# Kernel optimization log

Measured on AMD Instinct MI355X. Metric: run time of the kernel, lower is better.

Reference implementation:

```python
import jax, jax.numpy as jnp
import numpy as np

IN_C, HID, L, NN, BS, OUT = 32, 128, 4, 64, 512, 3
N = NN * BS  # total graph vertices
EPS_LN = 1e-5
EPS_SM = 1e-16  # PyG softmax eps


def setup_inputs() -> dict:
    key = jax.random.key(0)
    ks = jax.random.split(key, 16)
    E = 524288
    x = jax.random.normal(ks[0], (N, IN_C), dtype=jnp.float32)
    edge_index = jax.random.randint(ks[1], (2, E), 0, N, dtype=jnp.int64)
    s = 0.1
    # first GAT layer (in -> hidden)
    W0 = jax.random.normal(ks[2], (IN_C, HID), dtype=jnp.float32) * s
    att_src0 = jax.random.normal(ks[3], (HID,), dtype=jnp.float32) * s
    att_dst0 = jax.random.normal(ks[4], (HID,), dtype=jnp.float32) * s
    bias0 = jnp.zeros((HID,), dtype=jnp.float32)
    # residual GAT layers (hidden -> hidden), stacked over L
    W_res = jax.random.normal(ks[5], (L, HID, HID), dtype=jnp.float32) * s
    att_src_res = jax.random.normal(ks[6], (L, HID), dtype=jnp.float32) * s
    att_dst_res = jax.random.normal(ks[7], (L, HID), dtype=jnp.float32) * s
    bias_res = jnp.zeros((L, HID), dtype=jnp.float32)
    gamma = jnp.ones((L, HID), dtype=jnp.float32)
    beta = jnp.zeros((L, HID), dtype=jnp.float32)
    # per-node predictor heads
    W1p = jax.random.normal(ks[8], (NN, HID, HID // 2), dtype=jnp.float32) * s
    W2p = jax.random.normal(ks[9], (NN, HID // 2, OUT), dtype=jnp.float32) * s
    return {"x": x, "edge_index": edge_index, "W0": W0, "att_src0": att_src0,
            "att_dst0": att_dst0, "bias0": bias0, "W_res": W_res,
            "att_src_res": att_src_res, "att_dst_res": att_dst_res,
            "bias_res": bias_res, "gamma": gamma, "beta": beta,
            "W1p": W1p, "W2p": W2p}


def _gat(x, src, dst, W, a_src, a_dst, b):
    # PyG GATConv, heads=1, negative_slope=0.2, self-loops already appended
    h = x @ W                                   # [N, H]
    a_s = (h * a_src).sum(-1)                   # [N]
    a_d = (h * a_dst).sum(-1)                   # [N]
    e = jax.nn.leaky_relu(a_s[src] + a_d[dst], 0.2)   # [E]
    m = jax.ops.segment_max(e, dst, num_segments=N)
    e = jnp.exp(e - m[dst])
    z = jax.ops.segment_sum(e, dst, num_segments=N)
    alpha = e / (z[dst] + EPS_SM)               # [E]
    out = jax.ops.segment_sum(h[src] * alpha[:, None], dst, num_segments=N)
    return out + b


def _layernorm(x, g, b):
    mu = x.mean(-1, keepdims=True)
    var = ((x - mu) ** 2).mean(-1, keepdims=True)
    return (x - mu) * jax.lax.rsqrt(var + EPS_LN) * g + b


def reference(x, edge_index, W0, att_src0, att_dst0, bias0, W_res,
              att_src_res, att_dst_res, bias_res, gamma, beta, W1p, W2p):
    loops = jnp.arange(N, dtype=edge_index.dtype)
    src = jnp.concatenate([edge_index[0], loops])
    dst = jnp.concatenate([edge_index[1], loops])
    # first GAT + relu
    h = jax.nn.relu(_gat(x, src, dst, W0, att_src0, att_dst0, bias0))
    # res+ blocks: h = h + conv(dropout(act(norm(h))))  (dropout=identity, eval)
    for i in range(L):
        t = jax.nn.relu(_layernorm(h, gamma[i], beta[i]))
        t = _gat(t, src, dst, W_res[i], att_src_res[i], att_dst_res[i], bias_res[i])
        h = h + t
    h = jax.nn.relu(_layernorm(h, gamma[0], beta[0]))
    # per-node predictor heads
    h = h.reshape(NN, BS, HID)
    t = jax.nn.relu(jnp.einsum('nbh,nhk->nbk', h, W1p))
    logits = jnp.einsum('nbk,nko->nbo', t, W2p)
    return jax.nn.softmax(logits, axis=-1)   # softmax over class dim (dim=1 per node slice)
```

## Files before the change

### kernel.cpp

```cpp
#include <hip/hip_runtime.h>
#include <math.h>

#define NND   32768
#define HIDD  128
#define NHEAD 64
#define BSS   512
#define OUTC  3

typedef _Float16 half_t;
typedef __attribute__((ext_vector_type(8))) _Float16 half8;
typedef __attribute__((ext_vector_type(4))) float f32x4;

__global__ __launch_bounds__(256) void prep_kernel(const float* __restrict__ W0,
        const float* __restrict__ W_res, const float* __restrict__ W1p,
        const float* __restrict__ as0, const float* __restrict__ ad0,
        const float* __restrict__ as_res, const float* __restrict__ ad_res,
        const float* __restrict__ x,
        half_t* __restrict__ Wh, half_t* __restrict__ W1h, half_t* __restrict__ W0t,
        float* __restrict__ wvec, half_t* __restrict__ xh, int* __restrict__ counts) {
    int b = blockIdx.x, tid = threadIdx.x;
    if (b < 64) {
        __shared__ float tile[32][33];
        int l = b >> 4, t = b & 15;
        int k0 = (t >> 2) * 32, n0 = (t & 3) * 32;
        const float* src = W_res + (size_t)l * 128 * 128;
        half_t* dst = Wh + (size_t)l * 128 * 128;
        int c = tid & 31, r0 = tid >> 5;
#pragma unroll
        for (int i = 0; i < 4; ++i) tile[r0 + i * 8][c] = src[(size_t)(k0 + r0 + i * 8) * 128 + n0 + c];
        __syncthreads();
#pragma unroll
        for (int i = 0; i < 4; ++i) dst[(size_t)(n0 + r0 + i * 8) * 128 + k0 + c] = (half_t)tile[c][r0 + i * 8];
    } else if (b < 576) {
        __shared__ float tile[32][33];
        int bb = b - 64, head = bb >> 3, t = bb & 7;
        int k0 = (t >> 1) * 32, n0 = (t & 1) * 32;
        const float* src = W1p + (size_t)head * 128 * 64;
        half_t* dst = W1h + (size_t)head * 64 * 128;
        int c = tid & 31, r0 = tid >> 5;
#pragma unroll
        for (int i = 0; i < 4; ++i) tile[r0 + i * 8][c] = src[(size_t)(k0 + r0 + i * 8) * 64 + n0 + c];
        __syncthreads();
#pragma unroll
        for (int i = 0; i < 4; ++i) dst[(size_t)(n0 + r0 + i * 8) * 128 + k0 + c] = (half_t)tile[c][r0 + i * 8];
    } else if (b == 576) {
        __shared__ float t0[32][129];
        for (int i = tid; i < 4096; i += 256) t0[i >> 7][i & 127] = W0[i];
        __syncthreads();
        for (int i = tid; i < 4096; i += 256) { int n = i >> 5, k = i & 31; W0t[n * 32 + k] = (half_t)t0[k][n]; }
    } else if (b == 577) {
        for (int task = tid; task < 1088; task += 256) {
            const float* row; const float* att; int slot, sd;
            if (task < 64) {
                int k = task >> 1; sd = task & 1;
                row = W0 + k * 128; att = sd ? ad0 : as0; slot = k;
            } else {
                int tt = task - 64; int l = 1 + tt / 256; int r = tt % 256;
                int k = r >> 1; sd = r & 1;
                row = W_res + (size_t)(l - 1) * 16384 + k * 128;
                att = (sd ? ad_res : as_res) + (l - 1) * 128;
                slot = l * 128 + k;
            }
            float s = 0.f;
            for (int n = 0; n < 128; ++n) s += row[n] * att[n];
            (sd ? wvec + 640 : wvec)[slot] = s;
        }
    } else if (b < 1090) {
        int b2 = b - 578;
        const float* xs = x + (size_t)b2 * 64 * 32;
        half_t* xd = xh + (size_t)b2 * 64 * 32;
        for (int i = tid; i < 1024; i += 256) {
            float2 v = ((const float2*)xs)[i];
            union { unsigned u; half_t h[2]; } cv;
            cv.h[0] = (half_t)v.x; cv.h[1] = (half_t)v.y;
            ((unsigned*)xd)[i] = cv.u;
        }
    } else {
        int b3 = b - 1090;
        ((int4*)counts)[b3 * 256 + tid] = make_int4(0, 0, 0, 0);
    }
}

__global__ __launch_bounds__(256) void a0_kernel(const half_t* __restrict__ xh,
                                                 const float* __restrict__ wvec,
                                                 float* __restrict__ a_s, float* __restrict__ a_d) {
    __shared__ float ws0[32], wd0[32];
    int tid = threadIdx.x;
    if (tid < 32) { ws0[tid] = wvec[tid]; wd0[tid] = wvec[640 + tid]; }
    __syncthreads();
    int g = blockIdx.x * 256 + tid;
    int node = g >> 2, part = g & 3;
    half8 xv = *(const half8*)&xh[(size_t)node * 32 + part * 8];
    float s = 0.f, d2 = 0.f;
#pragma unroll
    for (int j = 0; j < 8; ++j) { float f = (float)xv[j]; s += f * ws0[part * 8 + j]; d2 += f * wd0[part * 8 + j]; }
    s += __shfl_xor(s, 1); s += __shfl_xor(s, 2);
    d2 += __shfl_xor(d2, 1); d2 += __shfl_xor(d2, 2);
    if (part == 0) { a_s[node] = s; a_d[node] = d2; }
}

__global__ void count_kernel(const int* __restrict__ ei, int E,
                             int* __restrict__ counts, int* __restrict__ rank) {
    int j = blockIdx.x * 256 + threadIdx.x;
    int Etot = E + NND;
    if (j >= Etot) return;
    int dst = (j < E) ? ei[E + j] : (j - E);
    rank[j] = atomicAdd(&counts[dst], 1);
}

__global__ __launch_bounds__(1024) void scan_kernel(const int* __restrict__ counts,
                                                    int* __restrict__ off) {
    __shared__ int sums[1024];
    int tid = threadIdx.x;
    int base = tid * 32;
    int tmp[32];
    int run = 0;
#pragma unroll
    for (int i = 0; i < 8; ++i) {
        int4 c4 = *(const int4*)&counts[base + i * 4];
        tmp[i*4+0] = run; run += c4.x;
        tmp[i*4+1] = run; run += c4.y;
        tmp[i*4+2] = run; run += c4.z;
        tmp[i*4+3] = run; run += c4.w;
    }
    sums[tid] = run;
    __syncthreads();
    for (int d = 1; d < 1024; d <<= 1) {
        int v = (tid >= d) ? sums[tid - d] : 0;
        __syncthreads();
        sums[tid] += v;
        __syncthreads();
    }
    int ebase = (tid == 0) ? 0 : sums[tid - 1];
#pragma unroll
    for (int i = 0; i < 32; ++i) off[base + i] = ebase + tmp[i];
    if (tid == 1023) off[NND] = sums[1023];
}

__global__ void fill_kernel(const int* __restrict__ ei, int E,
                            const int* __restrict__ off, const int* __restrict__ rank,
                            int* __restrict__ csr_src) {
    int j = blockIdx.x * 256 + threadIdx.x;
    int Etot = E + NND;
    if (j >= Etot) return;
    int src, dst;
    if (j < E) { src = ei[j]; dst = ei[E + j]; }
    else       { src = j - E; dst = j - E; }
    csr_src[off[dst] + rank[j]] = src;
}

__global__ __launch_bounds__(256) void agg0_kernel(const half_t* __restrict__ xh,
        const float* __restrict__ a_s, const float* __restrict__ a_dv,
        const int* __restrict__ csr_src, const int* __restrict__ off,
        half_t* __restrict__ P) {
    int d = (blockIdx.x * 256 + threadIdx.x) >> 6;
    int lane = threadIdx.x & 63;
    int q = lane >> 4, r15 = lane & 15;
    int beg = off[d], end = off[d + 1];
    float adv = a_dv[d];
    float pz = 0.f, a0 = 0.f, a1 = 0.f;
    for (int base = beg; base < end; base += 64) {
        int j = base + lane;
        int s = 0; float p = 0.f;
        if (j < end) {
            s = csr_src[j];
            float t = a_s[s] + adv;
            t = (t > 0.f) ? t : 0.2f * t;
            p = __expf(t);
        }
        pz += p;
        int cnt = end - base; if (cnt > 64) cnt = 64;
        int full = cnt & ~15;
        int k4 = 0;
        for (; k4 < full; k4 += 16) {
            int s0 = __shfl(s, k4 + q);      float p0 = __shfl(p, k4 + q);
            int s1 = __shfl(s, k4 + 4 + q);  float p1 = __shfl(p, k4 + 4 + q);
            int s2 = __shfl(s, k4 + 8 + q);  float p2 = __shfl(p, k4 + 8 + q);
            int s3 = __shfl(s, k4 + 12 + q); float p3 = __shfl(p, k4 + 12 + q);
            union { unsigned u; half_t h[2]; } u0, u1, u2, u3;
            u0.u = *(const unsigned*)&xh[(size_t)s0 * 32 + r15 * 2];
            u1.u = *(const unsigned*)&xh[(size_t)s1 * 32 + r15 * 2];
            u2.u = *(const unsigned*)&xh[(size_t)s2 * 32 + r15 * 2];
            u3.u = *(const unsigned*)&xh[(size_t)s3 * 32 + r15 * 2];
            a0 += p0 * (float)u0.h[0] + p1 * (float)u1.h[0] + p2 * (float)u2.h[0] + p3 * (float)u3.h[0];
            a1 += p0 * (float)u0.h[1] + p1 * (float)u1.h[1] + p2 * (float)u2.h[1] + p3 * (float)u3.h[1];
        }
        for (; k4 < cnt; k4 += 4) {
            int s0 = __shfl(s, k4 + q); float p0 = __shfl(p, k4 + q);
            union { unsigned u; half_t h[2]; } u0;
            u0.u = *(const unsigned*)&xh[(size_t)s0 * 32 + r15 * 2];
            a0 += p0 * (float)u0.h[0]; a1 += p0 * (float)u0.h[1];
        }
    }
#pragma unroll
    for (int o = 32; o; o >>= 1) pz += __shfl_xor(pz, o);
    a0 += __shfl_xor(a0, 16); a0 += __shfl_xor(a0, 32);
    a1 += __shfl_xor(a1, 16); a1 += __shfl_xor(a1, 32);
    if (q == 0) {
        float inv = 1.f / (pz + 1e-16f);
        union { unsigned u; half_t h[2]; } w;
        w.h[0] = (half_t)(a0 * inv); w.h[1] = (half_t)(a1 * inv);
        *(unsigned*)&P[(size_t)d * 32 + r15 * 2] = w.u;
    }
}

__global__ __launch_bounds__(256) void agg_kernel(const half_t* __restrict__ F,
        const float* __restrict__ a_s, const float* __restrict__ a_dv,
        const int* __restrict__ csr_src, const int* __restrict__ off,
        half_t* __restrict__ P) {
    int d = (blockIdx.x * 256 + threadIdx.x) >> 6;
    int lane = threadIdx.x & 63;
    int q = lane >> 4, r15 = lane & 15;
    int beg = off[d], end = off[d + 1];
    float adv = a_dv[d];
    float pz = 0.f;
    float acc[8] = {0.f,0.f,0.f,0.f,0.f,0.f,0.f,0.f};
    for (int base = beg; base < end; base += 64) {
        int j = base + lane;
        int s = 0; float p = 0.f;
        if (j < end) {
            s = csr_src[j];
            float t = a_s[s] + adv;
            t = (t > 0.f) ? t : 0.2f * t;
            p = __expf(t);
        }
        pz += p;
        int cnt = end - base; if (cnt > 64) cnt = 64;
        int full = cnt & ~15;
        int k4 = 0;
        for (; k4 < full; k4 += 16) {
            int s0 = __shfl(s, k4 + q);      float p0 = __shfl(p, k4 + q);
            int s1 = __shfl(s, k4 + 4 + q);  float p1 = __shfl(p, k4 + 4 + q);
            int s2 = __shfl(s, k4 + 8 + q);  float p2 = __shfl(p, k4 + 8 + q);
            int s3 = __shfl(s, k4 + 12 + q); float p3 = __shfl(p, k4 + 12 + q);
            half8 h0 = *(const half8*)&F[(size_t)s0 * HIDD + r15 * 8];
            half8 h1 = *(const half8*)&F[(size_t)s1 * HIDD + r15 * 8];
            half8 h2 = *(const half8*)&F[(size_t)s2 * HIDD + r15 * 8];
            half8 h3 = *(const half8*)&F[(size_t)s3 * HIDD + r15 * 8];
#pragma unroll
            for (int i = 0; i < 8; ++i) acc[i] += p0 * (float)h0[i];
#pragma unroll
            for (int i = 0; i < 8; ++i) acc[i] += p1 * (float)h1[i];
#pragma unroll
            for (int i = 0; i < 8; ++i) acc[i] += p2 * (float)h2[i];
#pragma unroll
            for (int i = 0; i < 8; ++i) acc[i] += p3 * (float)h3[i];
        }
        for (; k4 < cnt; k4 += 4) {
            int s0 = __shfl(s, k4 + q); float p0 = __shfl(p, k4 + q);
            half8 h0 = *(const half8*)&F[(size_t)s0 * HIDD + r15 * 8];
#pragma unroll
            for (int i = 0; i < 8; ++i) acc[i] += p0 * (float)h0[i];
        }
    }
#pragma unroll
    for (int o = 32; o; o >>= 1) pz += __shfl_xor(pz, o);
#pragma unroll
    for (int i = 0; i < 8; ++i) {
        acc[i] += __shfl_xor(acc[i], 16);
        acc[i] += __shfl_xor(acc[i], 32);
    }
    if (q == 0) {
        float inv = 1.f / (pz + 1e-16f);
        union { int4 v; half_t hh[8]; } u;
#pragma unroll
        for (int i = 0; i < 8; ++i) u.hh[i] = (half_t)(acc[i] * inv);
        *(int4*)&P[(size_t)d * HIDD + r15 * 8] = u.v;
    }
}

template <int K, bool RES>
__global__ __launch_bounds__(256) void gemm_kernel(const half_t* __restrict__ P,
        const half_t* __restrict__ Whl, const float* __restrict__ bias,
        float* __restrict__ Hbuf, half_t* __restrict__ Th,
        const float* __restrict__ gamma, const float* __restrict__ beta,
        const float* __restrict__ wsn, const float* __restrict__ wdn,
        float* __restrict__ a_s, float* __restrict__ a_d) {
    constexpr int KP = K + 8;
    __shared__ half_t Wt[128 * KP];
    __shared__ half_t OutT[64 * HIDD];
    int tid = threadIdx.x;
    int n0 = blockIdx.x * 64;
    for (int i = tid; i < 128 * (K / 8); i += 256) {
        int n = i / (K / 8), c = i % (K / 8);
        *(int4*)&Wt[n * KP + c * 8] = *(const int4*)&Whl[(size_t)n * K + c * 8];
    }
    int wv = tid >> 6, lane = tid & 63;
    int q = lane >> 4, r15 = lane & 15;
    half8 afrag[K / 32];
    int nodeA = n0 + wv * 16 + r15;
#pragma unroll
    for (int s = 0; s < K / 32; ++s)
        afrag[s] = *(const half8*)&P[(size_t)nodeA * K + s * 32 + q * 8];
    __syncthreads();
    f32x4 acc[8];
#pragma unroll
    for (int ct = 0; ct < 8; ++ct) {
        f32x4 c = {0.f, 0.f, 0.f, 0.f};
#pragma unroll
        for (int s = 0; s < K / 32; ++s) {
            half8 bfrag = *(const half8*)&Wt[(ct * 16 + r15) * KP + s * 32 + q * 8];
            c = __builtin_amdgcn_mfma_f32_16x16x32_f16(afrag[s], bfrag, c, 0, 0, 0);
        }
        acc[ct] = c;
    }
    int nodeD = n0 + wv * 16 + q * 4;
    float v[8][4];
#pragma unroll
    for (int ct = 0; ct < 8; ++ct) {
        int ch = ct * 16 + r15;
        float bv = bias[ch];
#pragma unroll
        for (int r = 0; r < 4; ++r) {
            float x2 = acc[ct][r] + bv;
            if (RES) x2 += Hbuf[(size_t)(nodeD + r) * HIDD + ch];
            else     x2 = fmaxf(x2, 0.f);
            v[ct][r] = x2;
            Hbuf[(size_t)(nodeD + r) * HIDD + ch] = x2;
        }
    }
    float sum[4] = {0.f,0.f,0.f,0.f};
#pragma unroll
    for (int ct = 0; ct < 8; ++ct)
#pragma unroll
        for (int r = 0; r < 4; ++r) sum[r] += v[ct][r];
#pragma unroll
    for (int o = 8; o; o >>= 1)
#pragma unroll
        for (int r = 0; r < 4; ++r) sum[r] += __shfl_xor(sum[r], o);
    float mu[4], var[4] = {0.f,0.f,0.f,0.f};
#pragma unroll
    for (int r = 0; r < 4; ++r) mu[r] = sum[r] * (1.f / HIDD);
#pragma unroll
    for (int ct = 0; ct < 8; ++ct)
#pragma unroll
        for (int r = 0; r < 4; ++r) { float dx = v[ct][r] - mu[r]; var[r] += dx * dx; }
#pragma unroll
    for (int o = 8; o; o >>= 1)
#pragma unroll
        for (int r = 0; r < 4; ++r) var[r] += __shfl_xor(var[r], o);
    float rs[4];
#pragma unroll
    for (int r = 0; r < 4; ++r) rs[r] = rsqrtf(var[r] * (1.f / HIDD) + 1e-5f);
    float asn[4] = {0.f,0.f,0.f,0.f}, adn[4] = {0.f,0.f,0.f,0.f};
#pragma unroll
    for (int ct = 0; ct < 8; ++ct) {
        int ch = ct * 16 + r15;
        float g = gamma[ch], be = beta[ch], wsv = wsn[ch], wdv = wdn[ch];
#pragma unroll
        for (int r = 0; r < 4; ++r) {
            float t = fmaxf((v[ct][r] - mu[r]) * rs[r] * g + be, 0.f);
            OutT[(wv * 16 + q * 4 + r) * HIDD + ch] = (half_t)t;
            asn[r] += t * wsv;
            adn[r] += t * wdv;
        }
    }
#pragma unroll
    for (int o = 8; o; o >>= 1)
#pragma unroll
        for (int r = 0; r < 4; ++r) { asn[r] += __shfl_xor(asn[r], o); adn[r] += __shfl_xor(adn[r], o); }
    if (r15 == 0) {
#pragma unroll
        for (int r = 0; r < 4; ++r) { a_s[nodeD + r] = asn[r]; a_d[nodeD + r] = adn[r]; }
    }
    __syncthreads();
    const int4* srcp = (const int4*)OutT;
    int4* dstp = (int4*)&Th[(size_t)n0 * HIDD];
    for (int i = tid; i < 64 * HIDD * 2 / 16; i += 256)
        dstp[i] = srcp[i];
}

__global__ __launch_bounds__(256) void gemm_last_kernel(const half_t* __restrict__ P,
        const half_t* __restrict__ Whl, const float* __restrict__ bias,
        const float* __restrict__ Hbuf,
        const float* __restrict__ gamma, const float* __restrict__ beta,
        const half_t* __restrict__ W1h, const float* __restrict__ W2p,
        float* __restrict__ out) {
    __shared__ half_t Wt[128 * 136];
    __shared__ half_t OutT[64 * HIDD];
    int tid = threadIdx.x;
    int n0 = blockIdx.x * 64;
    for (int i = tid; i < 128 * 16; i += 256) {
        int n = i >> 4, c = i & 15;
        *(int4*)&Wt[n * 136 + c * 8] = *(const int4*)&Whl[(size_t)n * 128 + c * 8];
    }
    int wv = tid >> 6, lane = tid & 63;
    int q = lane >> 4, r15 = lane & 15;
    half8 afrag[4];
    int nodeA = n0 + wv * 16 + r15;
#pragma unroll
    for (int s = 0; s < 4; ++s)
        afrag[s] = *(const half8*)&P[(size_t)nodeA * HIDD + s * 32 + q * 8];
    __syncthreads();
    f32x4 acc[8];
#pragma unroll
    for (int ct = 0; ct < 8; ++ct) {
        f32x4 c = {0.f, 0.f, 0.f, 0.f};
#pragma unroll
        for (int s = 0; s < 4; ++s) {
            half8 bfrag = *(const half8*)&Wt[(ct * 16 + r15) * 136 + s * 32 + q * 8];
            c = __builtin_amdgcn_mfma_f32_16x16x32_f16(afrag[s], bfrag, c, 0, 0, 0);
        }
        acc[ct] = c;
    }
    int nodeD = n0 + wv * 16 + q * 4;
    float v[8][4];
#pragma unroll
    for (int ct = 0; ct < 8; ++ct) {
        int ch = ct * 16 + r15;
        float bv = bias[ch];
#pragma unroll
        for (int r = 0; r < 4; ++r)
            v[ct][r] = acc[ct][r] + bv + Hbuf[(size_t)(nodeD + r) * HIDD + ch];
    }
    float sum[4] = {0.f,0.f,0.f,0.f};
#pragma unroll
    for (int ct = 0; ct < 8; ++ct)
#pragma unroll
        for (int r = 0; r < 4; ++r) sum[r] += v[ct][r];
#pragma unroll
    for (int o = 8; o; o >>= 1)
#pragma unroll
        for (int r = 0; r < 4; ++r) sum[r] += __shfl_xor(sum[r], o);
    float mu[4], var[4] = {0.f,0.f,0.f,0.f};
#pragma unroll
    for (int r = 0; r < 4; ++r) mu[r] = sum[r] * (1.f / HIDD);
#pragma unroll
    for (int ct = 0; ct < 8; ++ct)
#pragma unroll
        for (int r = 0; r < 4; ++r) { float dx = v[ct][r] - mu[r]; var[r] += dx * dx; }
#pragma unroll
    for (int o = 8; o; o >>= 1)
#pragma unroll
        for (int r = 0; r < 4; ++r) var[r] += __shfl_xor(var[r], o);
    float rs[4];
#pragma unroll
    for (int r = 0; r < 4; ++r) rs[r] = rsqrtf(var[r] * (1.f / HIDD) + 1e-5f);
#pragma unroll
    for (int ct = 0; ct < 8; ++ct) {
        int ch = ct * 16 + r15;
        float g = gamma[ch], be = beta[ch];
#pragma unroll
        for (int r = 0; r < 4; ++r) {
            float t = fmaxf((v[ct][r] - mu[r]) * rs[r] * g + be, 0.f);
            OutT[(wv * 16 + q * 4 + r) * HIDD + ch] = (half_t)t;
        }
    }
    __syncthreads();
    int head = n0 >> 9;
    const half_t* W1g = W1h + (size_t)head * 64 * 128;
    half8 pa[4];
#pragma unroll
    for (int s = 0; s < 4; ++s)
        pa[s] = *(const half8*)&OutT[(wv * 16 + r15) * HIDD + s * 32 + q * 8];
    float lg[3][4];
#pragma unroll
    for (int o = 0; o < 3; ++o)
#pragma unroll
        for (int r = 0; r < 4; ++r) lg[o][r] = 0.f;
#pragma unroll
    for (int ct2 = 0; ct2 < 4; ++ct2) {
        int n2 = ct2 * 16 + r15;
        f32x4 c = {0.f, 0.f, 0.f, 0.f};
#pragma unroll
        for (int s = 0; s < 4; ++s) {
            half8 bfrag = *(const half8*)&W1g[(size_t)n2 * 128 + s * 32 + q * 8];
            c = __builtin_amdgcn_mfma_f32_16x16x32_f16(pa[s], bfrag, c, 0, 0, 0);
        }
        float w2a = W2p[(size_t)head * 192 + n2 * 3 + 0];
        float w2b = W2p[(size_t)head * 192 + n2 * 3 + 1];
        float w2c = W2p[(size_t)head * 192 + n2 * 3 + 2];
#pragma unroll
        for (int r = 0; r < 4; ++r) {
            float t = fmaxf(c[r], 0.f);
            lg[0][r] += t * w2a;
            lg[1][r] += t * w2b;
            lg[2][r] += t * w2c;
        }
    }
#pragma unroll
    for (int o = 8; o; o >>= 1)
#pragma unroll
        for (int oo = 0; oo < 3; ++oo)
#pragma unroll
            for (int r = 0; r < 4; ++r) lg[oo][r] += __shfl_xor(lg[oo][r], o);
    if (r15 == 0) {
#pragma unroll
        for (int r = 0; r < 4; ++r) {
            int node = nodeD + r;
            float l0 = lg[0][r], l1 = lg[1][r], l2 = lg[2][r];
            float mx = fmaxf(l0, fmaxf(l1, l2));
            float e0 = __expf(l0 - mx), e1 = __expf(l1 - mx), e2 = __expf(l2 - mx);
            float inv = 1.f / (e0 + e1 + e2);
            float* op = out + (size_t)node * OUTC;
            op[0] = e0 * inv; op[1] = e1 * inv; op[2] = e2 * inv;
        }
    }
}

extern "C" void kernel_launch(void* const* d_in, const int* in_sizes, int n_in,
                              void* d_out, int out_size, void* d_ws, size_t ws_size,
                              hipStream_t stream) {
    const float* x        = (const float*)d_in[0];
    const int*   ei       = (const int*)d_in[1];
    const float* W0       = (const float*)d_in[2];
    const float* att_src0 = (const float*)d_in[3];
    const float* att_dst0 = (const float*)d_in[4];
    const float* bias0    = (const float*)d_in[5];
    const float* W_res    = (const float*)d_in[6];
    const float* as_res   = (const float*)d_in[7];
    const float* ad_res   = (const float*)d_in[8];
    const float* b_res    = (const float*)d_in[9];
    const float* gamma    = (const float*)d_in[10];
    const float* beta     = (const float*)d_in[11];
    const float* W1p      = (const float*)d_in[12];
    const float* W2p      = (const float*)d_in[13];
    float* out = (float*)d_out;

    int E = in_sizes[1] / 2;
    int Etot = E + NND;

    char* p = (char*)d_ws;
    auto alloc = [&](size_t bytes) { void* r = (void*)p; p += (bytes + 255) & ~(size_t)255; return r; };
    int*    counts  = (int*)alloc((size_t)NND * 4);
    int*    off     = (int*)alloc((size_t)(NND + 1) * 4);
    int*    rank    = (int*)alloc((size_t)Etot * 4);
    int*    csr_src = (int*)alloc((size_t)Etot * 4);
    half_t* xh      = (half_t*)alloc((size_t)NND * 32 * 2);
    half_t* Pbuf    = (half_t*)alloc((size_t)NND * HIDD * 2);
    half_t* Th      = (half_t*)alloc((size_t)NND * HIDD * 2);
    float*  Hbuf    = (float*)alloc((size_t)NND * HIDD * 4);
    float*  a_s     = (float*)alloc((size_t)NND * 4);
    float*  a_d     = (float*)alloc((size_t)NND * 4);
    half_t* Wh      = (half_t*)alloc((size_t)4 * HIDD * HIDD * 2);
    half_t* W1h     = (half_t*)alloc((size_t)NHEAD * 64 * HIDD * 2);
    half_t* W0t     = (half_t*)alloc((size_t)HIDD * 32 * 2);
    float*  wvec    = (float*)alloc((size_t)1280 * 4);

    int egrid = (Etot + 255) / 256;

    prep_kernel<<<1122, 256, 0, stream>>>(W0, W_res, W1p, att_src0, att_dst0,
                                          as_res, ad_res, x, Wh, W1h, W0t, wvec, xh, counts);
    a0_kernel<<<512, 256, 0, stream>>>(xh, wvec, a_s, a_d);
    count_kernel<<<egrid, 256, 0, stream>>>(ei, E, counts, rank);
    scan_kernel<<<1, 1024, 0, stream>>>(counts, off);
    fill_kernel<<<egrid, 256, 0, stream>>>(ei, E, off, rank, csr_src);

    agg0_kernel<<<NND / 4, 256, 0, stream>>>(xh, a_s, a_d, csr_src, off, Pbuf);
    gemm_kernel<32, false><<<NND / 64, 256, 0, stream>>>(Pbuf, W0t, bias0, Hbuf, Th,
        gamma, beta, wvec + 128, wvec + 640 + 128, a_s, a_d);

    for (int i = 0; i < 3; ++i) {
        agg_kernel<<<NND / 4, 256, 0, stream>>>(Th, a_s, a_d, csr_src, off, Pbuf);
        gemm_kernel<128, true><<<NND / 64, 256, 0, stream>>>(Pbuf, Wh + (size_t)i * 16384,
            b_res + i * HIDD, Hbuf, Th,
            gamma + (i + 1) * HIDD, beta + (i + 1) * HIDD,
            wvec + (i + 2) * 128, wvec + 640 + (i + 2) * 128, a_s, a_d);
    }

    agg_kernel<<<NND / 4, 256, 0, stream>>>(Th, a_s, a_d, csr_src, off, Pbuf);
    gemm_last_kernel<<<NND / 64, 256, 0, stream>>>(Pbuf, Wh + (size_t)3 * 16384,
        b_res + 3 * HIDD, Hbuf, gamma, beta, W1h, W2p, out);
}
```

Baseline: 302.5 us.

## Store residual stream in fp16, restage GEMM epilogue via LDS, fuse prep kernels

The residual hidden state buffer moves from fp32 to fp16, halving its read and write traffic in every GEMM epilogue. The epilogue now stages MFMA accumulators through shared memory (reusing the weight tile space) so each thread handles 8 contiguous channels of a node with vectorized loads and stores, instead of strided scalar accesses. The edge count pass is folded into prep_kernel (with counts zeroed by a memset), and fill plus a0 are merged into one launch, removing two launches. Keeping the residual in fp16 across five layers adds rounding error to the accumulated state.

```diff
diff --git a/kernel.cpp b/kernel.cpp
--- a/kernel.cpp
+++ b/kernel.cpp
@@ -15,9 +15,10 @@
         const float* __restrict__ W_res, const float* __restrict__ W1p,
         const float* __restrict__ as0, const float* __restrict__ ad0,
         const float* __restrict__ as_res, const float* __restrict__ ad_res,
-        const float* __restrict__ x,
+        const float* __restrict__ x, const int* __restrict__ ei, int E,
         half_t* __restrict__ Wh, half_t* __restrict__ W1h, half_t* __restrict__ W0t,
-        float* __restrict__ wvec, half_t* __restrict__ xh, int* __restrict__ counts) {
+        float* __restrict__ wvec, half_t* __restrict__ xh,
+        int* __restrict__ counts, int* __restrict__ rank) {
     int b = blockIdx.x, tid = threadIdx.x;
     if (b < 64) {
         __shared__ float tile[32][33];
@@ -76,36 +77,12 @@
             ((unsigned*)xd)[i] = cv.u;
         }
     } else {
-        int b3 = b - 1090;
-        ((int4*)counts)[b3 * 256 + tid] = make_int4(0, 0, 0, 0);
-    }
-}
-
-__global__ __launch_bounds__(256) void a0_kernel(const half_t* __restrict__ xh,
-                                                 const float* __restrict__ wvec,
-                                                 float* __restrict__ a_s, float* __restrict__ a_d) {
-    __shared__ float ws0[32], wd0[32];
-    int tid = threadIdx.x;
-    if (tid < 32) { ws0[tid] = wvec[tid]; wd0[tid] = wvec[640 + tid]; }
-    __syncthreads();
-    int g = blockIdx.x * 256 + tid;
-    int node = g >> 2, part = g & 3;
-    half8 xv = *(const half8*)&xh[(size_t)node * 32 + part * 8];
-    float s = 0.f, d2 = 0.f;
-#pragma unroll
-    for (int j = 0; j < 8; ++j) { float f = (float)xv[j]; s += f * ws0[part * 8 + j]; d2 += f * wd0[part * 8 + j]; }
-    s += __shfl_xor(s, 1); s += __shfl_xor(s, 2);
-    d2 += __shfl_xor(d2, 1); d2 += __shfl_xor(d2, 2);
-    if (part == 0) { a_s[node] = s; a_d[node] = d2; }
-}
-
-__global__ void count_kernel(const int* __restrict__ ei, int E,
-                             int* __restrict__ counts, int* __restrict__ rank) {
-    int j = blockIdx.x * 256 + threadIdx.x;
-    int Etot = E + NND;
-    if (j >= Etot) return;
-    int dst = (j < E) ? ei[E + j] : (j - E);
-    rank[j] = atomicAdd(&counts[dst], 1);
+        int j = (b - 1090) * 256 + tid;
+        int Etot = E + NND;
+        if (j >= Etot) return;
+        int dst = (j < E) ? ei[E + j] : (j - E);
+        rank[j] = atomicAdd(&counts[dst], 1);
+    }
 }
 
 __global__ __launch_bounds__(1024) void scan_kernel(const int* __restrict__ counts,
@@ -137,16 +114,33 @@
     if (tid == 1023) off[NND] = sums[1023];
 }
 
-__global__ void fill_kernel(const int* __restrict__ ei, int E,
-                            const int* __restrict__ off, const int* __restrict__ rank,
-                            int* __restrict__ csr_src) {
-    int j = blockIdx.x * 256 + threadIdx.x;
-    int Etot = E + NND;
-    if (j >= Etot) return;
-    int src, dst;
-    if (j < E) { src = ei[j]; dst = ei[E + j]; }
-    else       { src = j - E; dst = j - E; }
-    csr_src[off[dst] + rank[j]] = src;
+__global__ __launch_bounds__(256) void fill_a0_kernel(const int* __restrict__ ei, int E, int egrid,
+        const int* __restrict__ off, const int* __restrict__ rank, int* __restrict__ csr_src,
+        const half_t* __restrict__ xh, const float* __restrict__ wvec,
+        float* __restrict__ a_s, float* __restrict__ a_d) {
+    int b = blockIdx.x, tid = threadIdx.x;
+    if (b < egrid) {
+        int j = b * 256 + tid;
+        int Etot = E + NND;
+        if (j >= Etot) return;
+        int src, dst;
+        if (j < E) { src = ei[j]; dst = ei[E + j]; }
+        else       { src = j - E; dst = j - E; }
+        csr_src[off[dst] + rank[j]] = src;
+    } else {
+        __shared__ float ws0[32], wd0[32];
+        if (tid < 32) { ws0[tid] = wvec[tid]; wd0[tid] = wvec[640 + tid]; }
+        __syncthreads();
+        int g = (b - egrid) * 256 + tid;
+        int node = g >> 2, part = g & 3;
+        half8 xv = *(const half8*)&xh[(size_t)node * 32 + part * 8];
+        float s = 0.f, d2 = 0.f;
+#pragma unroll
+        for (int j = 0; j < 8; ++j) { float f = (float)xv[j]; s += f * ws0[part * 8 + j]; d2 += f * wd0[part * 8 + j]; }
+        s += __shfl_xor(s, 1); s += __shfl_xor(s, 2);
+        d2 += __shfl_xor(d2, 1); d2 += __shfl_xor(d2, 2);
+        if (part == 0) { a_s[node] = s; a_d[node] = d2; }
+    }
 }
 
 __global__ __launch_bounds__(256) void agg0_kernel(const half_t* __restrict__ xh,
@@ -272,18 +266,21 @@
 template <int K, bool RES>
 __global__ __launch_bounds__(256) void gemm_kernel(const half_t* __restrict__ P,
         const half_t* __restrict__ Whl, const float* __restrict__ bias,
-        float* __restrict__ Hbuf, half_t* __restrict__ Th,
+        half_t* __restrict__ Hh, half_t* __restrict__ Th,
         const float* __restrict__ gamma, const float* __restrict__ beta,
         const float* __restrict__ wsn, const float* __restrict__ wdn,
         float* __restrict__ a_s, float* __restrict__ a_d) {
     constexpr int KP = K + 8;
-    __shared__ half_t Wt[128 * KP];
-    __shared__ half_t OutT[64 * HIDD];
+    constexpr int WB = 128 * KP * 2;
+    constexpr int VB = 64 * 132 * 4;
+    __shared__ __align__(16) char smraw[(WB > VB) ? WB : VB];
+    half_t* w = (half_t*)smraw;
+    float* vv = (float*)smraw;
     int tid = threadIdx.x;
     int n0 = blockIdx.x * 64;
     for (int i = tid; i < 128 * (K / 8); i += 256) {
         int n = i / (K / 8), c = i % (K / 8);
-        *(int4*)&Wt[n * KP + c * 8] = *(const int4*)&Whl[(size_t)n * K + c * 8];
+        *(int4*)&w[n * KP + c * 8] = *(const int4*)&Whl[(size_t)n * K + c * 8];
     }
     int wv = tid >> 6, lane = tid & 63;
     int q = lane >> 4, r15 = lane & 15;
@@ -299,90 +296,90 @@
         f32x4 c = {0.f, 0.f, 0.f, 0.f};
 #pragma unroll
         for (int s = 0; s < K / 32; ++s) {
-            half8 bfrag = *(const half8*)&Wt[(ct * 16 + r15) * KP + s * 32 + q * 8];
+            half8 bfrag = *(const half8*)&w[(ct * 16 + r15) * KP + s * 32 + q * 8];
             c = __builtin_amdgcn_mfma_f32_16x16x32_f16(afrag[s], bfrag, c, 0, 0, 0);
         }
         acc[ct] = c;
     }
-    int nodeD = n0 + wv * 16 + q * 4;
-    float v[8][4];
-#pragma unroll
-    for (int ct = 0; ct < 8; ++ct) {
-        int ch = ct * 16 + r15;
-        float bv = bias[ch];
-#pragma unroll
-        for (int r = 0; r < 4; ++r) {
-            float x2 = acc[ct][r] + bv;
-            if (RES) x2 += Hbuf[(size_t)(nodeD + r) * HIDD + ch];
-            else     x2 = fmaxf(x2, 0.f);
-            v[ct][r] = x2;
-            Hbuf[(size_t)(nodeD + r) * HIDD + ch] = x2;
-        }
-    }
-    float sum[4] = {0.f,0.f,0.f,0.f};
+    __syncthreads();
 #pragma unroll
     for (int ct = 0; ct < 8; ++ct)
 #pragma unroll
-        for (int r = 0; r < 4; ++r) sum[r] += v[ct][r];
-#pragma unroll
-    for (int o = 8; o; o >>= 1)
-#pragma unroll
-        for (int r = 0; r < 4; ++r) sum[r] += __shfl_xor(sum[r], o);
-    float mu[4], var[4] = {0.f,0.f,0.f,0.f};
-#pragma unroll
-    for (int r = 0; r < 4; ++r) mu[r] = sum[r] * (1.f / HIDD);
-#pragma unroll
-    for (int ct = 0; ct < 8; ++ct)
-#pragma unroll
-        for (int r = 0; r < 4; ++r) { float dx = v[ct][r] - mu[r]; var[r] += dx * dx; }
-#pragma unroll
-    for (int o = 8; o; o >>= 1)
-#pragma unroll
-        for (int r = 0; r < 4; ++r) var[r] += __shfl_xor(var[r], o);
-    float rs[4];
-#pragma unroll
-    for (int r = 0; r < 4; ++r) rs[r] = rsqrtf(var[r] * (1.f / HIDD) + 1e-5f);
-    float asn[4] = {0.f,0.f,0.f,0.f}, adn[4] = {0.f,0.f,0.f,0.f};
-#pragma unroll
-    for (int ct = 0; ct < 8; ++ct) {
-        int ch = ct * 16 + r15;
-        float g = gamma[ch], be = beta[ch], wsv = wsn[ch], wdv = wdn[ch];
-#pragma unroll
-        for (int r = 0; r < 4; ++r) {
-            float t = fmaxf((v[ct][r] - mu[r]) * rs[r] * g + be, 0.f);
-            OutT[(wv * 16 + q * 4 + r) * HIDD + ch] = (half_t)t;
-            asn[r] += t * wsv;
-            adn[r] += t * wdv;
-        }
-    }
-#pragma unroll
-    for (int o = 8; o; o >>= 1)
-#pragma unroll
-        for (int r = 0; r < 4; ++r) { asn[r] += __shfl_xor(asn[r], o); adn[r] += __shfl_xor(adn[r], o); }
-    if (r15 == 0) {
-#pragma unroll
-        for (int r = 0; r < 4; ++r) { a_s[nodeD + r] = asn[r]; a_d[nodeD + r] = adn[r]; }
-    }
-    __syncthreads();
-    const int4* srcp = (const int4*)OutT;
-    int4* dstp = (int4*)&Th[(size_t)n0 * HIDD];
-    for (int i = tid; i < 64 * HIDD * 2 / 16; i += 256)
-        dstp[i] = srcp[i];
+        for (int r = 0; r < 4; ++r)
+            vv[(wv * 16 + q * 4 + r) * 132 + ct * 16 + r15] = acc[ct][r];
+    __syncthreads();
+    int grp = tid >> 4, sub = tid & 15;
+    float4 bi0 = *(const float4*)&bias[sub * 8],  bi1 = *(const float4*)&bias[sub * 8 + 4];
+    float4 g0  = *(const float4*)&gamma[sub * 8], g1  = *(const float4*)&gamma[sub * 8 + 4];
+    float4 be0 = *(const float4*)&beta[sub * 8],  be1 = *(const float4*)&beta[sub * 8 + 4];
+    float4 ws0 = *(const float4*)&wsn[sub * 8],   ws1 = *(const float4*)&wsn[sub * 8 + 4];
+    float4 wd0 = *(const float4*)&wdn[sub * 8],   wd1 = *(const float4*)&wdn[sub * 8 + 4];
+    float bi[8] = {bi0.x,bi0.y,bi0.z,bi0.w,bi1.x,bi1.y,bi1.z,bi1.w};
+    float gg[8] = {g0.x,g0.y,g0.z,g0.w,g1.x,g1.y,g1.z,g1.w};
+    float be[8] = {be0.x,be0.y,be0.z,be0.w,be1.x,be1.y,be1.z,be1.w};
+    float ws[8] = {ws0.x,ws0.y,ws0.z,ws0.w,ws1.x,ws1.y,ws1.z,ws1.w};
+    float wd[8] = {wd0.x,wd0.y,wd0.z,wd0.w,wd1.x,wd1.y,wd1.z,wd1.w};
+#pragma unroll
+    for (int pp = 0; pp < 4; ++pp) {
+        int nl = grp + pp * 16;
+        int node = n0 + nl;
+        float v8[8];
+#pragma unroll
+        for (int j = 0; j < 8; ++j) v8[j] = vv[nl * 132 + sub * 8 + j] + bi[j];
+        if (RES) {
+            half8 hold = *(const half8*)&Hh[(size_t)node * HIDD + sub * 8];
+#pragma unroll
+            for (int j = 0; j < 8; ++j) v8[j] += (float)hold[j];
+        } else {
+#pragma unroll
+            for (int j = 0; j < 8; ++j) v8[j] = fmaxf(v8[j], 0.f);
+        }
+        union { int4 i4; half_t h[8]; } hw;
+#pragma unroll
+        for (int j = 0; j < 8; ++j) hw.h[j] = (half_t)v8[j];
+        *(int4*)&Hh[(size_t)node * HIDD + sub * 8] = hw.i4;
+        float sum = 0.f;
+#pragma unroll
+        for (int j = 0; j < 8; ++j) sum += v8[j];
+#pragma unroll
+        for (int o = 8; o; o >>= 1) sum += __shfl_xor(sum, o);
+        float mu = sum * (1.f / HIDD);
+        float var = 0.f;
+#pragma unroll
+        for (int j = 0; j < 8; ++j) { float dx = v8[j] - mu; var += dx * dx; }
+#pragma unroll
+        for (int o = 8; o; o >>= 1) var += __shfl_xor(var, o);
+        float rs = rsqrtf(var * (1.f / HIDD) + 1e-5f);
+        union { int4 i4; half_t h[8]; } tw;
+        float asn = 0.f, adn = 0.f;
+#pragma unroll
+        for (int j = 0; j < 8; ++j) {
+            float t = fmaxf((v8[j] - mu) * rs * gg[j] + be[j], 0.f);
+            tw.h[j] = (half_t)t;
+            asn += t * ws[j];
+            adn += t * wd[j];
+        }
+        *(int4*)&Th[(size_t)node * HIDD + sub * 8] = tw.i4;
+#pragma unroll
+        for (int o = 8; o; o >>= 1) { asn += __shfl_xor(asn, o); adn += __shfl_xor(adn, o); }
+        if (sub == 0) { a_s[node] = asn; a_d[node] = adn; }
+    }
 }
 
 __global__ __launch_bounds__(256) void gemm_last_kernel(const half_t* __restrict__ P,
         const half_t* __restrict__ Whl, const float* __restrict__ bias,
-        const float* __restrict__ Hbuf,
+        const half_t* __restrict__ Hh,
         const float* __restrict__ gamma, const float* __restrict__ beta,
         const half_t* __restrict__ W1h, const float* __restrict__ W2p,
         float* __restrict__ out) {
-    __shared__ half_t Wt[128 * 136];
-    __shared__ half_t OutT[64 * HIDD];
+    __shared__ __align__(16) char smraw[128 * 136 * 2];
+    half_t* w = (half_t*)smraw;
+    float* vv = (float*)smraw;
     int tid = threadIdx.x;
     int n0 = blockIdx.x * 64;
     for (int i = tid; i < 128 * 16; i += 256) {
         int n = i >> 4, c = i & 15;
-        *(int4*)&Wt[n * 136 + c * 8] = *(const int4*)&Whl[(size_t)n * 128 + c * 8];
+        *(int4*)&w[n * 136 + c * 8] = *(const int4*)&Whl[(size_t)n * 128 + c * 8];
     }
     int wv = tid >> 6, lane = tid & 63;
     int q = lane >> 4, r15 = lane & 15;
@@ -398,53 +395,58 @@
         f32x4 c = {0.f, 0.f, 0.f, 0.f};
 #pragma unroll
         for (int s = 0; s < 4; ++s) {
-            half8 bfrag = *(const half8*)&Wt[(ct * 16 + r15) * 136 + s * 32 + q * 8];
+            half8 bfrag = *(const half8*)&w[(ct * 16 + r15) * 136 + s * 32 + q * 8];
             c = __builtin_amdgcn_mfma_f32_16x16x32_f16(afrag[s], bfrag, c, 0, 0, 0);
         }
         acc[ct] = c;
     }
-    int nodeD = n0 + wv * 16 + q * 4;
-    float v[8][4];
-#pragma unroll
-    for (int ct = 0; ct < 8; ++ct) {
-        int ch = ct * 16 + r15;
-        float bv = bias[ch];
+    __syncthreads();
+#pragma unroll
+    for (int ct = 0; ct < 8; ++ct)
 #pragma unroll
         for (int r = 0; r < 4; ++r)
-            v[ct][r] = acc[ct][r] + bv + Hbuf[(size_t)(nodeD + r) * HIDD + ch];
-    }
-    float sum[4] = {0.f,0.f,0.f,0.f};
-#pragma unroll
-    for (int ct = 0; ct < 8; ++ct)
-#pragma unroll
-        for (int r = 0; r < 4; ++r) sum[r] += v[ct][r];
-#pragma unroll
-    for (int o = 8; o; o >>= 1)
-#pragma unroll
-        for (int r = 0; r < 4; ++r) sum[r] += __shfl_xor(sum[r], o);
-    float mu[4], var[4] = {0.f,0.f,0.f,0.f};
-#pragma unroll
-    for (int r = 0; r < 4; ++r) mu[r] = sum[r] * (1.f / HIDD);
-#pragma unroll
-    for (int ct = 0; ct < 8; ++ct)
-#pragma unroll
-        for (int r = 0; r < 4; ++r) { float dx = v[ct][r] - mu[r]; var[r] += dx * dx; }
-#pragma unroll
-    for (int o = 8; o; o >>= 1)
-#pragma unroll
-        for (int r = 0; r < 4; ++r) var[r] += __shfl_xor(var[r], o);
-    float rs[4];
-#pragma unroll
-    for (int r = 0; r < 4; ++r) rs[r] = rsqrtf(var[r] * (1.f / HIDD) + 1e-5f);
-#pragma unroll
-    for (int ct = 0; ct < 8; ++ct) {
-        int ch = ct * 16 + r15;
-        float g = gamma[ch], be = beta[ch];
-#pragma unroll
-        for (int r = 0; r < 4; ++r) {
-            float t = fmaxf((v[ct][r] - mu[r]) * rs[r] * g + be, 0.f);
-            OutT[(wv * 16 + q * 4 + r) * HIDD + ch] = (half_t)t;
-        }
+            vv[(wv * 16 + q * 4 + r) * 132 + ct * 16 + r15] = acc[ct][r];
+    __syncthreads();
+    int grp = tid >> 4, sub = tid & 15;
+    float4 bi0 = *(const float4*)&bias[sub * 8],  bi1 = *(const float4*)&bias[sub * 8 + 4];
+    float4 g0  = *(const float4*)&gamma[sub * 8], g1  = *(const float4*)&gamma[sub * 8 + 4];
+    float4 be0 = *(const float4*)&beta[sub * 8],  be1 = *(const float4*)&beta[sub * 8 + 4];
+    float bi[8] = {bi0.x,bi0.y,bi0.z,bi0.w,bi1.x,bi1.y,bi1.z,bi1.w};
+    float gg[8] = {g0.x,g0.y,g0.z,g0.w,g1.x,g1.y,g1.z,g1.w};
+    float be[8] = {be0.x,be0.y,be0.z,be0.w,be1.x,be1.y,be1.z,be1.w};
+    half_t tv[4][8];
+#pragma unroll
+    for (int pp = 0; pp < 4; ++pp) {
+        int nl = grp + pp * 16;
+        int node = n0 + nl;
+        float v8[8];
+        half8 hold = *(const half8*)&Hh[(size_t)node * HIDD + sub * 8];
+#pragma unroll
+        for (int j = 0; j < 8; ++j) v8[j] = vv[nl * 132 + sub * 8 + j] + bi[j] + (float)hold[j];
+        float sum = 0.f;
+#pragma unroll
+        for (int j = 0; j < 8; ++j) sum += v8[j];
+#pragma unroll
+        for (int o = 8; o; o >>= 1) sum += __shfl_xor(sum, o);
+        float mu = sum * (1.f / HIDD);
+        float var = 0.f;
+#pragma unroll
+        for (int j = 0; j < 8; ++j) { float dx = v8[j] - mu; var += dx * dx; }
+#pragma unroll
+        for (int o = 8; o; o >>= 1) var += __shfl_xor(var, o);
+        float rs = rsqrtf(var * (1.f / HIDD) + 1e-5f);
+#pragma unroll
+        for (int j = 0; j < 8; ++j)
+            tv[pp][j] = (half_t)fmaxf((v8[j] - mu) * rs * gg[j] + be[j], 0.f);
+    }
+    __syncthreads();
+#pragma unroll
+    for (int pp = 0; pp < 4; ++pp) {
+        int nl = grp + pp * 16;
+        union { int4 i4; half_t h[8]; } u;
+#pragma unroll
+        for (int j = 0; j < 8; ++j) u.h[j] = tv[pp][j];
+        *(int4*)&w[nl * 136 + sub * 8] = u.i4;
     }
     __syncthreads();
     int head = n0 >> 9;
@@ -452,7 +454,7 @@
     half8 pa[4];
 #pragma unroll
     for (int s = 0; s < 4; ++s)
-        pa[s] = *(const half8*)&OutT[(wv * 16 + r15) * HIDD + s * 32 + q * 8];
+        pa[s] = *(const half8*)&w[(wv * 16 + r15) * 136 + s * 32 + q * 8];
     float lg[3][4];
 #pragma unroll
     for (int o = 0; o < 3; ++o)
@@ -485,14 +487,14 @@
 #pragma unroll
             for (int r = 0; r < 4; ++r) lg[oo][r] += __shfl_xor(lg[oo][r], o);
     if (r15 == 0) {
+        int nodeD = n0 + wv * 16 + q * 4;
 #pragma unroll
         for (int r = 0; r < 4; ++r) {
-            int node = nodeD + r;
             float l0 = lg[0][r], l1 = lg[1][r], l2 = lg[2][r];
             float mx = fmaxf(l0, fmaxf(l1, l2));
             float e0 = __expf(l0 - mx), e1 = __expf(l1 - mx), e2 = __expf(l2 - mx);
             float inv = 1.f / (e0 + e1 + e2);
-            float* op = out + (size_t)node * OUTC;
+            float* op = out + (size_t)(nodeD + r) * OUTC;
             op[0] = e0 * inv; op[1] = e1 * inv; op[2] = e2 * inv;
         }
     }
@@ -529,7 +531,7 @@
     half_t* xh      = (half_t*)alloc((size_t)NND * 32 * 2);
     half_t* Pbuf    = (half_t*)alloc((size_t)NND * HIDD * 2);
     half_t* Th      = (half_t*)alloc((size_t)NND * HIDD * 2);
-    float*  Hbuf    = (float*)alloc((size_t)NND * HIDD * 4);
+    half_t* Hh      = (half_t*)alloc((size_t)NND * HIDD * 2);
     float*  a_s     = (float*)alloc((size_t)NND * 4);
     float*  a_d     = (float*)alloc((size_t)NND * 4);
     half_t* Wh      = (half_t*)alloc((size_t)4 * HIDD * HIDD * 2);
@@ -539,26 +541,26 @@
 
     int egrid = (Etot + 255) / 256;
 
-    prep_kernel<<<1122, 256, 0, stream>>>(W0, W_res, W1p, att_src0, att_dst0,
-                                          as_res, ad_res, x, Wh, W1h, W0t, wvec, xh, counts);
-    a0_kernel<<<512, 256, 0, stream>>>(xh, wvec, a_s, a_d);
-    count_kernel<<<egrid, 256, 0, stream>>>(ei, E, counts, rank);
+    hipMemsetAsync(counts, 0, (size_t)NND * 4, stream);
+    prep_kernel<<<1090 + egrid, 256, 0, stream>>>(W0, W_res, W1p, att_src0, att_dst0,
+        as_res, ad_res, x, ei, E, Wh, W1h, W0t, wvec, xh, counts, rank);
     scan_kernel<<<1, 1024, 0, stream>>>(counts, off);
-    fill_kernel<<<egrid, 256, 0, stream>>>(ei, E, off, rank, csr_src);
+    fill_a0_kernel<<<egrid + 512, 256, 0, stream>>>(ei, E, egrid, off, rank, csr_src,
+                                                    xh, wvec, a_s, a_d);
 
     agg0_kernel<<<NND / 4, 256, 0, stream>>>(xh, a_s, a_d, csr_src, off, Pbuf);
-    gemm_kernel<32, false><<<NND / 64, 256, 0, stream>>>(Pbuf, W0t, bias0, Hbuf, Th,
+    gemm_kernel<32, false><<<NND / 64, 256, 0, stream>>>(Pbuf, W0t, bias0, Hh, Th,
         gamma, beta, wvec + 128, wvec + 640 + 128, a_s, a_d);
 
     for (int i = 0; i < 3; ++i) {
         agg_kernel<<<NND / 4, 256, 0, stream>>>(Th, a_s, a_d, csr_src, off, Pbuf);
         gemm_kernel<128, true><<<NND / 64, 256, 0, stream>>>(Pbuf, Wh + (size_t)i * 16384,
-            b_res + i * HIDD, Hbuf, Th,
+            b_res + i * HIDD, Hh, Th,
             gamma + (i + 1) * HIDD, beta + (i + 1) * HIDD,
             wvec + (i + 2) * 128, wvec + 640 + (i + 2) * 128, a_s, a_d);
     }
 
     agg_kernel<<<NND / 4, 256, 0, stream>>>(Th, a_s, a_d, csr_src, off, Pbuf);
     gemm_last_kernel<<<NND / 64, 256, 0, stream>>>(Pbuf, Wh + (size_t)3 * 16384,
-        b_res + 3 * HIDD, Hbuf, gamma, beta, W1h, W2p, out);
-}
+        b_res + 3 * HIDD, Hh, gamma, beta, W1h, W2p, out);
+}
```

Result: faster. 293.4 us (-3.0%).
